# Kernel optimization log

Measured on AMD Instinct MI355X. Metric: run time of the kernel, lower is better.

Reference implementation:

```python
import jax, jax.numpy as jnp
import numpy as np

ALPHA = 1.0
ARAP_WEIGHT = 1.0
B, N, K, LATENT, HIDDEN = 16, 20000, 16, 256, 1024


def setup_inputs() -> dict:
    key = jax.random.key(0)
    ks = jax.random.split(key, 8)
    code = jax.random.normal(ks[0], (B, LATENT), jnp.float32)
    W1 = jax.random.normal(ks[1], (LATENT, HIDDEN), jnp.float32) / np.sqrt(LATENT)
    b1 = jnp.zeros((HIDDEN,), jnp.float32)
    W2 = jax.random.normal(ks[2], (HIDDEN, N * 3), jnp.float32) / np.sqrt(HIDDEN)
    b2 = jnp.zeros((N * 3,), jnp.float32)
    xyz1 = jax.random.normal(ks[3], (B, N, 3), jnp.float32)
    weightMatrix = jax.random.uniform(ks[4], (N, K), jnp.float32)
    area = jax.random.uniform(ks[5], (N,), jnp.float32)
    neighborsMatrix = jax.random.randint(ks[6], (N, K), 0, N, jnp.int32)
    numNeighbors = jax.random.randint(ks[7], (N,), 1, K + 1, jnp.int32)
    return {"code": code, "W1": W1, "b1": b1, "W2": W2, "b2": b2,
            "xyz1": xyz1, "weightMatrix": weightMatrix, "area": area,
            "neighborsMatrix": neighborsMatrix, "numNeighbors": numNeighbors}


def _mean_energy(code, W1, b1, W2, b2, xyz1, weightMatrix, area,
                 neighborsMatrix, numNeighbors):
    # decoder: MLP latent -> hidden -> N*3, reshaped to [B,N,3]
    h = jax.nn.relu(code @ W1 + b1)
    recon = (h @ W2 + b2).reshape(B, N, 3)

    # mask out padded neighbor slots, fold into weights  [N,K]
    mask = (jnp.arange(K)[None, :] < numNeighbors[:, None]).astype(jnp.float32)
    wm = weightMatrix * mask

    # neighbor-gathered edge vectors: rest pose d, deformed dq  [B,N,K,3]
    d = xyz1[:, :, None, :] - xyz1[:, neighborsMatrix, :]
    dq = recon[:, :, None, :] - recon[:, neighborsMatrix, :]

    # per-vertex weighted covariance and best-fit rotation (Procrustes)
    S = jnp.einsum('nk,bnki,bnkj->bnij', wm, d, dq)          # [B,N,3,3]
    U, s, Vt = jnp.linalg.svd(S)
    V = jnp.swapaxes(Vt, -1, -2)
    Ut = jnp.swapaxes(U, -1, -2)
    det = jnp.linalg.det(V @ Ut)                              # [B,N]
    Vf = V.at[..., :, -1].multiply(jnp.sign(det)[..., None])  # reflection fix
    R = jax.lax.stop_gradient(Vf @ Ut)                        # R treated as constant

    resid = dq - jnp.einsum('bnij,bnkj->bnki', R, d)          # [B,N,K,3]
    e = (ARAP_WEIGHT * ALPHA) * area[None, :, None] * wm[None] \
        * jnp.sum(resid * resid, axis=-1)                     # [B,N,K]
    # torch.mean(torch.mean(e, 2), 1)
    return jnp.mean(e, axis=(1, 2))                           # [B]


def reference(code, W1, b1, W2, b2, xyz1, weightMatrix, area,
              neighborsMatrix, numNeighbors):
    meanEnergy = _mean_energy(code, W1, b1, W2, b2, xyz1, weightMatrix, area,
                              neighborsMatrix, numNeighbors)
    # meanEnergy.backward(ones) -> grad of sum(meanEnergy) wrt code
    code_grad = jax.grad(lambda c: jnp.sum(
        _mean_energy(c, W1, b1, W2, b2, xyz1, weightMatrix, area,
                     neighborsMatrix, numNeighbors)))(code)
    return (meanEnergy, code_grad)
```

## Files before the change

kernel.cpp:

```cpp
#include <hip/hip_runtime.h>

constexpr int B_ = 16;
constexpr int NV = 20000;
constexpr int KN = 16;
constexpr int LAT = 256;
constexpr int HID = 1024;
constexpr int N3 = 60000;
constexpr int RCAP = 64;
constexpr int NCHUNK = 8;
constexpr float INV_NK = 1.0f / (20000.0f * 16.0f);

constexpr size_t H_OFF      = 0;
constexpr size_t XQ_OFF     = H_OFF + B_ * HID;
constexpr size_t GRECON_OFF = XQ_OFF + (size_t)NV * 96;
constexpr size_t GH_OFF     = GRECON_OFF + (size_t)B_ * N3;
constexpr size_t OWNG_OFF   = GH_OFF + B_ * HID;
constexpr size_t GEDGE_OFF  = OWNG_OFF + (size_t)NV * 64;
constexpr size_t RCOUNT_OFF = GEDGE_OFF + (size_t)NV * KN * 64;
constexpr size_t RLIST_OFF  = RCOUNT_OFF + NV;
constexpr size_t PART_OFF   = RLIST_OFF + (size_t)NV * RCAP;

__device__ __forceinline__ void atomAddF(float* p, float v) {
  unsafeAtomicAdd(p, v);
}

__global__ __launch_bounds__(256) void k_prep(
    const float* __restrict__ xyz, const float* __restrict__ code,
    const float* __restrict__ W1, const float* __restrict__ b1,
    float* __restrict__ xq, float* __restrict__ h,
    float* __restrict__ gh, float* __restrict__ out,
    int* __restrict__ rcount) {
  const int bid = blockIdx.x, tid = threadIdx.x;
  if (bid < 938) {
    __shared__ float sm[64][17];
    const int n30 = bid * 64;
    {
      const int n3l = tid & 63, bq = tid >> 6;
      #pragma unroll
      for (int p = 0; p < 4; ++p) {
        int b = p * 4 + bq;
        if (n30 + n3l < N3) sm[n3l][b] = xyz[(size_t)b * N3 + n30 + n3l];
      }
    }
    __syncthreads();
    {
      const int b = tid & 15, nq = tid >> 4;
      #pragma unroll
      for (int p = 0; p < 4; ++p) {
        int n3 = n30 + p * 16 + nq;
        if (n3 < N3) {
          int n = n3 / 3, c = n3 - n * 3;
          xq[(size_t)n * 96 + c * 16 + b] = sm[p * 16 + nq][b];
        }
      }
    }
  } else if (bid < 1002) {
    int t = (bid - 938) * 256 + tid;
    int b = t >> 10, hd = t & 1023;
    const float* c = code + b * LAT;
    float acc = b1[hd];
    #pragma unroll 4
    for (int l = 0; l < LAT; ++l) acc += c[l] * W1[l * HID + hd];
    h[t] = fmaxf(acc, 0.0f);
  } else if (bid < 1006) {
    int base = (bid - 1002) * 4096 + tid;
    #pragma unroll
    for (int r = 0; r < 16; ++r) gh[base + r * 256] = 0.0f;
  } else if (bid == 1006) {
    for (int i = tid; i < B_ + B_ * LAT; i += 256) out[i] = 0.0f;
  } else {
    int i = (bid - 1007) * 256 + tid;
    if (i < NV) rcount[i] = 0;
  }
}

__global__ __launch_bounds__(256) void k_mlp2f(
    const float* __restrict__ h, const float* __restrict__ W2,
    float* __restrict__ part,
    const int* __restrict__ nbrs, const int* __restrict__ nnbr,
    int* __restrict__ rcount, int* __restrict__ rlist) {
  const int bid = blockIdx.x;
  const int tid = threadIdx.x;
  if (bid >= 472) {
    int e = (bid - 472) * 256 + tid;
    int n = e >> 4, k = e & 15;
    if (k < nnbr[n]) {
      int v = nbrs[e];
      int slot = atomicAdd(&rcount[v], 1);
      if (slot < RCAP) rlist[v * RCAP + slot] = e;
    }
    return;
  }
  const int bx = bid % 59, by = bid / 59;
  __shared__ float hs[16][128];
  const int hd0 = by * 128;
  #pragma unroll
  for (int r = 0; r < 8; ++r) {
    int idx = r * 256 + tid;
    int bb = idx >> 7, cc = idx & 127;
    hs[bb][cc] = h[bb * HID + hd0 + cc];
  }
  __syncthreads();

  const int j4 = bx * 1024 + tid * 4;
  if (j4 >= N3) return;

  float4 acc[16];
  #pragma unroll
  for (int b = 0; b < 16; ++b) acc[b] = make_float4(0.f, 0.f, 0.f, 0.f);

  const float* wp = W2 + (size_t)hd0 * N3 + j4;
  float4 w0 = *(const float4*)(wp);
  float4 w1 = *(const float4*)(wp + (size_t)N3);
  float4 w2 = *(const float4*)(wp + (size_t)2 * N3);
  float4 w3 = *(const float4*)(wp + (size_t)3 * N3);

  for (int g = 0; g < 32; ++g) {
    const float* np = wp + (size_t)4 * N3;
    float4 n0, n1, n2, n3;
    if (g < 31) {
      n0 = *(const float4*)(np);
      n1 = *(const float4*)(np + (size_t)N3);
      n2 = *(const float4*)(np + (size_t)2 * N3);
      n3 = *(const float4*)(np + (size_t)3 * N3);
    }
    #pragma unroll
    for (int b = 0; b < 16; ++b) {
      float4 hb = *(const float4*)&hs[b][g * 4];
      acc[b].x += hb.x * w0.x + hb.y * w1.x + hb.z * w2.x + hb.w * w3.x;
      acc[b].y += hb.x * w0.y + hb.y * w1.y + hb.z * w2.y + hb.w * w3.y;
      acc[b].z += hb.x * w0.z + hb.y * w1.z + hb.z * w2.z + hb.w * w3.z;
      acc[b].w += hb.x * w0.w + hb.y * w1.w + hb.z * w2.w + hb.w * w3.w;
    }
    wp = np; w0 = n0; w1 = n1; w2 = n2; w3 = n3;
  }

  float ac[4][16];
  #pragma unroll
  for (int b = 0; b < 16; ++b) {
    ac[0][b] = acc[b].x; ac[1][b] = acc[b].y;
    ac[2][b] = acc[b].z; ac[3][b] = acc[b].w;
  }
  float* pbase = part + ((size_t)by * N3 + j4) * 16;
  #pragma unroll
  for (int jj = 0; jj < 4; ++jj)
    #pragma unroll
    for (int q = 0; q < 4; ++q)
      *(float4*)(pbase + jj * 16 + q * 4) = make_float4(
          ac[jj][q*4+0], ac[jj][q*4+1], ac[jj][q*4+2], ac[jj][q*4+3]);
}

__global__ __launch_bounds__(256) void k_reduce(
    const float* __restrict__ part, const float* __restrict__ b2,
    float* __restrict__ xq) {
  int t = blockIdx.x * 256 + threadIdx.x;
  if (t >= N3 * 16 / 4) return;
  size_t pos = (size_t)t * 4;
  int j = t >> 2, bq = (t & 3) * 4;
  float4 s = *(const float4*)(part + pos);
  #pragma unroll
  for (int c = 1; c < NCHUNK; ++c) {
    float4 p = *(const float4*)(part + (size_t)c * N3 * 16 + pos);
    s.x += p.x; s.y += p.y; s.z += p.z; s.w += p.w;
  }
  float bias = b2[j];
  s.x += bias; s.y += bias; s.z += bias; s.w += bias;
  int n = j / 3, c = j - n * 3;
  *(float4*)(xq + (size_t)n * 96 + (3 + c) * 16 + bq) = s;
}

__global__ __launch_bounds__(256, 2) void k_rot(
    const float* __restrict__ xq,
    const float* __restrict__ wmat, const float* __restrict__ area,
    const int* __restrict__ nbrs, const int* __restrict__ nnbr,
    float* __restrict__ ownG, float* __restrict__ gEdge,
    float* __restrict__ energy) {
  __shared__ float red[64];
  const int tid = threadIdx.x;
  const int b = tid & 15, nl = tid >> 4;
  const int n = blockIdx.x * 16 + nl;
  const int nn = nnbr[n];
  const float ar = area[n];
  const float* xqn = xq + (size_t)n * 96 + b;
  const float x0 = xqn[0],  x1 = xqn[16], x2 = xqn[32];
  const float q0 = xqn[48], q1 = xqn[64], q2 = xqn[80];

  float dX[KN], dY[KN], dZ[KN], eX[KN], eY[KN], eZ[KN], wk[KN];
  float S00=0,S01=0,S02=0,S10=0,S11=0,S12=0,S20=0,S21=0,S22=0;
  #pragma unroll
  for (int k = 0; k < KN; ++k) {
    float w=0, dx=0, dy=0, dz=0, ex=0, ey=0, ez=0;
    if (k < nn) {
      int m = nbrs[n * KN + k];
      w = wmat[n * KN + k];
      const float* mp = xq + (size_t)m * 96 + b;
      dx = x0 - mp[0];  dy = x1 - mp[16]; dz = x2 - mp[32];
      ex = q0 - mp[48]; ey = q1 - mp[64]; ez = q2 - mp[80];
    }
    wk[k]=w; dX[k]=dx; dY[k]=dy; dZ[k]=dz; eX[k]=ex; eY[k]=ey; eZ[k]=ez;
    S00 += w*dx*ex; S01 += w*dx*ey; S02 += w*dx*ez;
    S10 += w*dy*ex; S11 += w*dy*ey; S12 += w*dy*ez;
    S20 += w*dz*ex; S21 += w*dz*ey; S22 += w*dz*ez;
  }

  float A00 = S00*S00 + S10*S10 + S20*S20;
  float A01 = S00*S01 + S10*S11 + S20*S21;
  float A02 = S00*S02 + S10*S12 + S20*S22;
  float A11 = S01*S01 + S11*S11 + S21*S21;
  float A12 = S01*S02 + S11*S12 + S21*S22;
  float A22 = S02*S02 + S12*S12 + S22*S22;
  float V00=1,V01=0,V02=0, V10=0,V11=1,V12=0, V20=0,V21=0,V22=1;

  auto rot = [&](float& app, float& aqq, float& apq, float& arp, float& arq,
                 float& vp0, float& vp1, float& vp2,
                 float& vq0, float& vq1, float& vq2) {
    float a = apq;
    if (fabsf(a) > 1e-37f) {
      float tau = (aqq - app) * 0.5f / a;
      float t = copysignf(1.0f, tau) / (fabsf(tau) + sqrtf(1.0f + tau * tau));
      float c = rsqrtf(1.0f + t * t);
      float s = t * c;
      float napp = c*c*app - 2.0f*s*c*a + s*s*aqq;
      float naqq = s*s*app + 2.0f*s*c*a + c*c*aqq;
      app = napp; aqq = naqq; apq = 0.0f;
      float rp = arp, rq = arq;
      arp = c*rp - s*rq; arq = s*rp + c*rq;
      float t0, t1;
      t0=vp0; t1=vq0; vp0 = c*t0 - s*t1; vq0 = s*t0 + c*t1;
      t0=vp1; t1=vq1; vp1 = c*t0 - s*t1; vq1 = s*t0 + c*t1;
      t0=vp2; t1=vq2; vp2 = c*t0 - s*t1; vq2 = s*t0 + c*t1;
    }
  };
  #pragma unroll
  for (int sweep = 0; sweep < 6; ++sweep) {
    rot(A00,A11,A01, A02,A12, V00,V10,V20, V01,V11,V21);
    rot(A00,A22,A02, A01,A12, V00,V10,V20, V02,V12,V22);
    rot(A11,A22,A12, A01,A02, V01,V11,V21, V02,V12,V22);
  }
  auto sw = [](float& a, float& c) { float t = a; a = c; c = t; };
  if (A00 < A11) { sw(A00,A11); sw(V00,V01); sw(V10,V11); sw(V20,V21); }
  if (A00 < A22) { sw(A00,A22); sw(V00,V02); sw(V10,V12); sw(V20,V22); }
  if (A11 < A22) { sw(A11,A22); sw(V01,V02); sw(V11,V12); sw(V21,V22); }

  float v1x=V00, v1y=V10, v1z=V20;
  float v2x=V01, v2y=V11, v2z=V21;

  float u1x = S00*v1x + S01*v1y + S02*v1z;
  float u1y = S10*v1x + S11*v1y + S12*v1z;
  float u1z = S20*v1x + S21*v1y + S22*v1z;
  float s1sq = u1x*u1x + u1y*u1y + u1z*u1z;
  if (s1sq > 1e-30f) { float r = rsqrtf(s1sq); u1x*=r; u1y*=r; u1z*=r; }
  else { u1x = 1.0f; u1y = 0.0f; u1z = 0.0f; }

  float u2x = S00*v2x + S01*v2y + S02*v2z;
  float u2y = S10*v2x + S11*v2y + S12*v2z;
  float u2z = S20*v2x + S21*v2y + S22*v2z;
  float pr = u2x*u1x + u2y*u1y + u2z*u1z;
  u2x -= pr*u1x; u2y -= pr*u1y; u2z -= pr*u1z;
  float s2sq = u2x*u2x + u2y*u2y + u2z*u2z;
  if (s2sq > 1e-12f * s1sq + 1e-30f) {
    float r = rsqrtf(s2sq); u2x*=r; u2y*=r; u2z*=r;
  } else {
    float ex_ = (fabsf(u1x) < 0.9f) ? 1.0f : 0.0f;
    float ey_ = 1.0f - ex_;
    float pp = ex_*u1x + ey_*u1y;
    u2x = ex_ - pp*u1x; u2y = ey_ - pp*u1y; u2z = -pp*u1z;
    float r = rsqrtf(u2x*u2x + u2y*u2y + u2z*u2z);
    u2x*=r; u2y*=r; u2z*=r;
  }
  float u3x = u1y*u2z - u1z*u2y, u3y = u1z*u2x - u1x*u2z, u3z = u1x*u2y - u1y*u2x;
  float v3x = v1y*v2z - v1z*v2y, v3y = v1z*v2x - v1x*v2z, v3z = v1x*v2y - v1y*v2x;

  float R00 = v1x*u1x + v2x*u2x + v3x*u3x;
  float R01 = v1x*u1y + v2x*u2y + v3x*u3y;
  float R02 = v1x*u1z + v2x*u2z + v3x*u3z;
  float R10 = v1y*u1x + v2y*u2x + v3y*u3x;
  float R11 = v1y*u1y + v2y*u2y + v3y*u3y;
  float R12 = v1y*u1z + v2y*u2z + v3y*u3z;
  float R20 = v1z*u1x + v2z*u2x + v3z*u3x;
  float R21 = v1z*u1y + v2z*u2y + v3z*u3y;
  float R22 = v1z*u1z + v2z*u2z + v3z*u3z;

  float esum = 0, go0 = 0, go1 = 0, go2 = 0;
  const float gf = 2.0f * ar * INV_NK;
  float* geb = gEdge + (size_t)n * 1024 + b * 4;
  #pragma unroll
  for (int k = 0; k < KN; ++k) {
    float w = wk[k];
    float dx = dX[k], dy = dY[k], dz = dZ[k];
    float rx = eX[k] - (R00*dx + R01*dy + R02*dz);
    float ry = eY[k] - (R10*dx + R11*dy + R12*dz);
    float rz = eZ[k] - (R20*dx + R21*dy + R22*dz);
    esum += w * (rx*rx + ry*ry + rz*rz);
    float gc = gf * w;
    float gx = gc*rx, gy = gc*ry, gz = gc*rz;
    go0 += gx; go1 += gy; go2 += gz;
    if (k < nn) {
      *(float4*)(geb + k * 64) = make_float4(gx, gy, gz, 0.0f);
    }
  }
  esum *= ar * INV_NK;

  *(float4*)(ownG + (size_t)n * 64 + b * 4) = make_float4(go0, go1, go2, 0.0f);

  esum += __shfl_down(esum, 32);
  esum += __shfl_down(esum, 16);
  int wave = tid >> 6, lane = tid & 63;
  if (lane < 16) red[wave * 16 + lane] = esum;
  __syncthreads();
  if (tid < 16) atomAddF(&energy[tid], red[tid] + red[16 + tid] + red[32 + tid] + red[48 + tid]);
}

__global__ __launch_bounds__(256) void k_scatter(
    const float* __restrict__ gEdge, const float* __restrict__ ownG,
    const int* __restrict__ rcount, const int* __restrict__ rlist,
    float* __restrict__ grecon) {
  int t = blockIdx.x * 256 + threadIdx.x;
  int v = t >> 4, b = t & 15;
  const float4 og = *(const float4*)(ownG + (size_t)v * 64 + b * 4);
  float g0 = og.x, g1 = og.y, g2 = og.z;
  int deg = min(rcount[v], RCAP);
  const int* rl = rlist + v * RCAP;
  int i = 0;
  for (; i + 3 < deg; i += 4) {
    int e0 = rl[i], e1 = rl[i + 1], e2 = rl[i + 2], e3 = rl[i + 3];
    float4 p0 = *(const float4*)(gEdge + (size_t)e0 * 64 + b * 4);
    float4 p1 = *(const float4*)(gEdge + (size_t)e1 * 64 + b * 4);
    float4 p2 = *(const float4*)(gEdge + (size_t)e2 * 64 + b * 4);
    float4 p3 = *(const float4*)(gEdge + (size_t)e3 * 64 + b * 4);
    g0 -= (p0.x + p1.x) + (p2.x + p3.x);
    g1 -= (p0.y + p1.y) + (p2.y + p3.y);
    g2 -= (p0.z + p1.z) + (p2.z + p3.z);
  }
  for (; i < deg; ++i) {
    int e = rl[i];
    float4 p = *(const float4*)(gEdge + (size_t)e * 64 + b * 4);
    g0 -= p.x; g1 -= p.y; g2 -= p.z;
  }
  float* gq = grecon + (size_t)b * N3 + v * 3;
  gq[0] = g0; gq[1] = g1; gq[2] = g2;
}

__global__ __launch_bounds__(256) void k_mlp2_bwd(
    const float* __restrict__ gr, const float* __restrict__ W2,
    float* __restrict__ gh) {
  const int tid = threadIdx.x;
  const int lane = tid & 63;
  const int wv = tid >> 6;
  const int laneJ = lane & 15, laneR = lane >> 4;
  const int row = blockIdx.y * 16 + wv * 4 + laneR;

  float acc[16];
  #pragma unroll
  for (int b = 0; b < 16; ++b) acc[b] = 0.0f;

  const int jbase = blockIdx.x * 64 + laneJ * 4;
  const float* w2r = W2 + (size_t)row * N3;

  for (int it = 0; it < 58; ++it) {
    int j = jbase + it * 1024;
    float4 w0 = *(const float4*)(w2r + j);
    #pragma unroll
    for (int b = 0; b < 16; ++b) {
      float4 g = *(const float4*)(gr + (size_t)b * N3 + j);
      acc[b] += g.x * w0.x + g.y * w0.y + g.z * w0.z + g.w * w0.w;
    }
  }
  {
    int j = jbase + 58 * 1024;
    if (j < N3) {
      float4 w0 = *(const float4*)(w2r + j);
      #pragma unroll
      for (int b = 0; b < 16; ++b) {
        float4 g = *(const float4*)(gr + (size_t)b * N3 + j);
        acc[b] += g.x * w0.x + g.y * w0.y + g.z * w0.z + g.w * w0.w;
      }
    }
  }

  #pragma unroll
  for (int m = 1; m <= 8; m <<= 1) {
    #pragma unroll
    for (int b = 0; b < 16; ++b) acc[b] += __shfl_xor(acc[b], m);
  }
  if (laneJ == 0) {
    #pragma unroll
    for (int b = 0; b < 16; ++b) atomAddF(&gh[b * HID + row], acc[b]);
  }
}

__global__ __launch_bounds__(256) void k_mlp1_bwd(
    const float* __restrict__ gh, const float* __restrict__ h,
    const float* __restrict__ W1, float* __restrict__ gcode) {
  __shared__ float gm[128];
  const int b = blockIdx.x;
  const int hd0 = blockIdx.y * 128;
  const int l = threadIdx.x;
  if (l < 128) {
    float g = gh[b * HID + hd0 + l];
    gm[l] = (h[b * HID + hd0 + l] > 0.0f) ? g : 0.0f;
  }
  __syncthreads();
  const float4* wp = (const float4*)(W1 + (size_t)l * HID + hd0);
  float acc = 0.0f;
  #pragma unroll
  for (int i = 0; i < 32; ++i) {
    float4 w4 = wp[i];
    acc += w4.x * gm[i*4+0] + w4.y * gm[i*4+1] + w4.z * gm[i*4+2] + w4.w * gm[i*4+3];
  }
  atomAddF(&gcode[b * LAT + l], acc);
}

extern "C" void kernel_launch(void* const* d_in, const int* in_sizes, int n_in,
                              void* d_out, int out_size, void* d_ws, size_t ws_size,
                              hipStream_t stream) {
  const float* code = (const float*)d_in[0];
  const float* W1   = (const float*)d_in[1];
  const float* b1   = (const float*)d_in[2];
  const float* W2   = (const float*)d_in[3];
  const float* b2   = (const float*)d_in[4];
  const float* xyz  = (const float*)d_in[5];
  const float* wmat = (const float*)d_in[6];
  const float* area = (const float*)d_in[7];
  const int* nbrs   = (const int*)d_in[8];
  const int* nnbr   = (const int*)d_in[9];

  float* out = (float*)d_out;
  float* ws = (float*)d_ws;
  float* h      = ws + H_OFF;
  float* xq     = ws + XQ_OFF;
  float* grecon = ws + GRECON_OFF;
  float* gh     = ws + GH_OFF;
  float* ownG   = ws + OWNG_OFF;
  float* gEdge  = ws + GEDGE_OFF;
  int*   rcount = (int*)(ws + RCOUNT_OFF);
  int*   rlist  = (int*)(ws + RLIST_OFF);
  float* part   = ws + PART_OFF;

  k_prep<<<dim3(1086), dim3(256), 0, stream>>>(xyz, code, W1, b1, xq, h, gh, out, rcount);
  k_mlp2f<<<dim3(472 + NV * KN / 256), dim3(256), 0, stream>>>(
      h, W2, part, nbrs, nnbr, rcount, rlist);
  k_reduce<<<dim3((N3 * 16 / 4 + 255) / 256), dim3(256), 0, stream>>>(part, b2, xq);
  k_rot<<<dim3(NV / 16), dim3(256), 0, stream>>>(
      xq, wmat, area, nbrs, nnbr, ownG, gEdge, out);
  k_scatter<<<dim3(NV * 16 / 256), dim3(256), 0, stream>>>(
      gEdge, ownG, rcount, rlist, grecon);
  k_mlp2_bwd<<<dim3(16, 64), dim3(256), 0, stream>>>(grecon, W2, gh);
  k_mlp1_bwd<<<dim3(B_, 8), dim3(256), 0, stream>>>(gh, h, W1, out + B_);
}
```

Baseline: 632.7 us.

## Stage grecon tiles in double-buffered LDS for MLP2 backward

```diff
diff --git a/kernel.cpp b/kernel.cpp
--- a/kernel.cpp
+++ b/kernel.cpp
@@ -344,36 +344,91 @@
 __global__ __launch_bounds__(256) void k_mlp2_bwd(
     const float* __restrict__ gr, const float* __restrict__ W2,
     float* __restrict__ gh) {
+  __shared__ float4 ldsA[16][64];
+  __shared__ float4 ldsB[16][64];
   const int tid = threadIdx.x;
   const int lane = tid & 63;
-  const int wv = tid >> 6;
+  const int wave = tid >> 6;
   const int laneJ = lane & 15, laneR = lane >> 4;
-  const int row = blockIdx.y * 16 + wv * 4 + laneR;
+  const int row = blockIdx.y * 16 + wave * 4 + laneR;
+  const int jlo = blockIdx.x * 15000;
+  const float* w2r = W2 + (size_t)row * N3;
+
+  int sb[4], sq[4];
+  #pragma unroll
+  for (int k = 0; k < 4; ++k) { int idx = k * 256 + tid; sb[k] = idx >> 6; sq[k] = idx & 63; }
 
   float acc[16];
   #pragma unroll
   for (int b = 0; b < 16; ++b) acc[b] = 0.0f;
 
-  const int jbase = blockIdx.x * 64 + laneJ * 4;
-  const float* w2r = W2 + (size_t)row * N3;
-
-  for (int it = 0; it < 58; ++it) {
-    int j = jbase + it * 1024;
-    float4 w0 = *(const float4*)(w2r + j);
-    #pragma unroll
-    for (int b = 0; b < 16; ++b) {
-      float4 g = *(const float4*)(gr + (size_t)b * N3 + j);
-      acc[b] += g.x * w0.x + g.y * w0.y + g.z * w0.z + g.w * w0.w;
-    }
-  }
-  {
-    int j = jbase + 58 * 1024;
-    if (j < N3) {
-      float4 w0 = *(const float4*)(w2r + j);
+  float4 (*cur)[64] = ldsA;
+  float4 (*nxt)[64] = ldsB;
+
+  #pragma unroll
+  for (int k = 0; k < 4; ++k)
+    cur[sb[k]][sq[k]] = *(const float4*)(gr + (size_t)sb[k] * N3 + jlo + sq[k] * 4);
+  __syncthreads();
+
+  for (int t = 0; t < 57; ++t) {
+    const int jbase = jlo + t * 256;
+    const int jn = jbase + 256;
+    float4 r0 = *(const float4*)(gr + (size_t)sb[0] * N3 + jn + sq[0] * 4);
+    float4 r1 = *(const float4*)(gr + (size_t)sb[1] * N3 + jn + sq[1] * 4);
+    float4 r2 = *(const float4*)(gr + (size_t)sb[2] * N3 + jn + sq[2] * 4);
+    float4 r3 = *(const float4*)(gr + (size_t)sb[3] * N3 + jn + sq[3] * 4);
+    #pragma unroll
+    for (int s = 0; s < 4; ++s) {
+      float4 w = *(const float4*)(w2r + jbase + s * 64 + laneJ * 4);
       #pragma unroll
       for (int b = 0; b < 16; ++b) {
-        float4 g = *(const float4*)(gr + (size_t)b * N3 + j);
-        acc[b] += g.x * w0.x + g.y * w0.y + g.z * w0.z + g.w * w0.w;
+        float4 g = cur[b][s * 16 + laneJ];
+        acc[b] += g.x * w.x + g.y * w.y + g.z * w.z + g.w * w.w;
+      }
+    }
+    nxt[sb[0]][sq[0]] = r0; nxt[sb[1]][sq[1]] = r1;
+    nxt[sb[2]][sq[2]] = r2; nxt[sb[3]][sq[3]] = r3;
+    __syncthreads();
+    float4 (*tmp)[64] = cur; cur = nxt; nxt = tmp;
+  }
+
+  {
+    const int jbase = jlo + 57 * 256;
+    const int jn = jbase + 256;
+    float4 r0, r1, r2, r3;
+    if (sq[0] < 38) r0 = *(const float4*)(gr + (size_t)sb[0] * N3 + jn + sq[0] * 4);
+    if (sq[1] < 38) r1 = *(const float4*)(gr + (size_t)sb[1] * N3 + jn + sq[1] * 4);
+    if (sq[2] < 38) r2 = *(const float4*)(gr + (size_t)sb[2] * N3 + jn + sq[2] * 4);
+    if (sq[3] < 38) r3 = *(const float4*)(gr + (size_t)sb[3] * N3 + jn + sq[3] * 4);
+    #pragma unroll
+    for (int s = 0; s < 4; ++s) {
+      float4 w = *(const float4*)(w2r + jbase + s * 64 + laneJ * 4);
+      #pragma unroll
+      for (int b = 0; b < 16; ++b) {
+        float4 g = cur[b][s * 16 + laneJ];
+        acc[b] += g.x * w.x + g.y * w.y + g.z * w.z + g.w * w.w;
+      }
+    }
+    if (sq[0] < 38) nxt[sb[0]][sq[0]] = r0;
+    if (sq[1] < 38) nxt[sb[1]][sq[1]] = r1;
+    if (sq[2] < 38) nxt[sb[2]][sq[2]] = r2;
+    if (sq[3] < 38) nxt[sb[3]][sq[3]] = r3;
+    __syncthreads();
+    float4 (*tmp)[64] = cur; cur = nxt; nxt = tmp;
+  }
+
+  {
+    const int jbase = jlo + 58 * 256;
+    #pragma unroll
+    for (int s = 0; s < 4; ++s) {
+      int jo = s * 64 + laneJ * 4;
+      if (jo < 152) {
+        float4 w = *(const float4*)(w2r + jbase + jo);
+        #pragma unroll
+        for (int b = 0; b < 16; ++b) {
+          float4 g = cur[b][s * 16 + laneJ];
+          acc[b] += g.x * w.x + g.y * w.y + g.z * w.z + g.w * w.w;
+        }
       }
     }
   }
@@ -445,6 +500,6 @@
       xq, wmat, area, nbrs, nnbr, ownG, gEdge, out);
   k_scatter<<<dim3(NV * 16 / 256), dim3(256), 0, stream>>>(
       gEdge, ownG, rcount, rlist, grecon);
-  k_mlp2_bwd<<<dim3(16, 64), dim3(256), 0, stream>>>(grecon, W2, gh);
+  k_mlp2_bwd<<<dim3(4, 64), dim3(256), 0, stream>>>(grecon, W2, gh);
   k_mlp1_bwd<<<dim3(B_, 8), dim3(256), 0, stream>>>(gh, h, W1, out + B_);
 }
```

New measurement: 636.4 us. About the same (+0.6%).
